# Performance work log

Hardware: AMD Instinct MI355X
Metric: run time of the kernel (lower is better)

Reference implementation:

```python
import jax, jax.numpy as jnp
import numpy as np

DIM = 64
HEADS = 8
P = 4  # polarizations
EPS = 1e-12


def _conv2d(x, w, b, groups):
    # x: [N,C,H,W], w: [O, C//groups, kh, kw] (torch OIHW), stride 1, SAME padding
    y = jax.lax.conv_general_dilated(
        x, w, window_strides=(1, 1), padding='SAME',
        dimension_numbers=('NCHW', 'OIHW', 'NCHW'), feature_group_count=groups)
    return y + b[None, :, None, None]


def setup_inputs() -> dict:
    key = jax.random.key(0)
    ks = jax.random.split(key, 12)
    B, C, H, W = 4, DIM, 128, 128
    s = 1.0 / np.sqrt(C)
    x_in = jax.random.normal(ks[0], (B * P, C, H, W), dtype=jnp.float32)
    mask = jax.random.uniform(ks[1], (B * P, C, H, W), dtype=jnp.float32)
    wq = jax.random.normal(ks[2], (C, C), dtype=jnp.float32) * s
    wk = jax.random.normal(ks[3], (C, C), dtype=jnp.float32) * s
    wv = jax.random.normal(ks[4], (C, C), dtype=jnp.float32) * s
    w_proj = jax.random.normal(ks[5], (C, C), dtype=jnp.float32) * s
    b_proj = jax.random.normal(ks[6], (C,), dtype=jnp.float32) * 0.01
    rescale = jnp.ones((HEADS, 1, 1), dtype=jnp.float32)
    dw_w = jax.random.normal(ks[7], (C, 1, 3, 3), dtype=jnp.float32) * (1.0 / 3.0)
    dw_b = jax.random.normal(ks[8], (C,), dtype=jnp.float32) * 0.01
    pw_w = jax.random.normal(ks[9], (C, C, 1, 1), dtype=jnp.float32) * s
    pw_b = jax.random.normal(ks[10], (C,), dtype=jnp.float32) * 0.01
    return {'x_in': x_in, 'mask': mask, 'wq': wq, 'wk': wk, 'wv': wv,
            'w_proj': w_proj, 'b_proj': b_proj, 'rescale': rescale,
            'dw_w': dw_w, 'dw_b': dw_b, 'pw_w': pw_w, 'pw_b': pw_b}


def reference(x_in, mask, wq, wk, wv, w_proj, b_proj, rescale, dw_w, dw_b, pw_w, pw_b):
    bp, c, h, w = x_in.shape
    b_num = bp // P
    dh = c // HEADS
    # 'b p c h w -> (b h w) p c'
    x = x_in.reshape(b_num, P, c, h, w).transpose(0, 3, 4, 1, 2).reshape(b_num * h * w, P, c)
    # torch Linear (no bias): x @ W.T
    q = jnp.einsum('bpc,dc->bpd', x, wq)
    k = jnp.einsum('bpc,dc->bpd', x, wk)
    v = jnp.einsum('bpc,dc->bpd', x, wv)
    # 'b p (h c) -> b h p c'
    q = q.reshape(-1, P, HEADS, dh).transpose(0, 2, 1, 3)
    k = k.reshape(-1, P, HEADS, dh).transpose(0, 2, 1, 3)
    v = v.reshape(-1, P, HEADS, dh).transpose(0, 2, 1, 3)
    # L2 normalize along head dim (torch F.normalize: clamp_min(eps))
    q = q / jnp.maximum(jnp.linalg.norm(q, axis=-1, keepdims=True), EPS)
    k = k / jnp.maximum(jnp.linalg.norm(k, axis=-1, keepdims=True), EPS)
    atten = jnp.einsum('bhpc,bhqc->bhpq', q, k) * rescale  # rescale: [heads,1,1]
    # mask branch: depthwise 3x3 -> GELU(exact) -> pointwise 1x1
    mg = _conv2d(mask, dw_w, dw_b, groups=c)
    mg = jax.nn.gelu(mg, approximate=False)
    mg = _conv2d(mg, pw_w, pw_b, groups=1)
    mg = mg.reshape(b_num, P, c, h, w).mean(axis=2)  # [b,p,h,w]
    mb = mg.transpose(0, 2, 3, 1).reshape(b_num * h * w, P)  # '(b h w) p'
    mask_bias = mb[:, None, :] - mb[:, :, None]  # [B, p, p]
    atten = atten + mask_bias[:, None, :, :]
    atten = jax.nn.softmax(atten, axis=-1)
    out = jnp.einsum('bhpq,bhqc->bhpc', atten, v)
    out = out.transpose(0, 2, 1, 3).reshape(-1, P, c)  # 'b h p c -> b p (h c)'
    out = jnp.einsum('bpc,dc->bpd', out, w_proj) + b_proj
    # '(b h w) p c -> b p c h w' -> [(b p), c, h, w]
    out = out.reshape(b_num, h, w, P, c).transpose(0, 3, 4, 1, 2)
    return out.reshape(b_num * P, c, h, w)
```

## Files before the change

kernel.cpp:

```cpp
#include <hip/hip_runtime.h>
#include <hip/hip_bf16.h>

#define HSZ 128
#define WSZ 128
#define HWSZ (HSZ*WSZ)
#define NB 4

#define OFF_MB 0

typedef unsigned short u16;
typedef __attribute__((ext_vector_type(8))) short bf16x8;
typedef __attribute__((ext_vector_type(4))) float f32x4;

__device__ __forceinline__ float bf2f(u16 u) {
    return __uint_as_float(((unsigned int)u) << 16);
}
__device__ __forceinline__ unsigned int cvt_pk_bf16(float lo, float hi) {
    __hip_bfloat162 h = __float22bfloat162_rn(make_float2(lo, hi));
    return *(unsigned int*)&h;
}
__device__ __forceinline__ u16 f2bf_bits(float f) {
    unsigned int x = __float_as_uint(f);
    return (u16)((x + 0x7fffu + ((x >> 16) & 1u)) >> 16);
}
__device__ __forceinline__ int sswz(int s) { return s ^ (s >> 3); }
__device__ __forceinline__ int qkv_idx(int t, int d) {
    return (t >> 2)*64 + ((((t & 3) + (t >> 2)) & 3) << 4) + d;
}
__device__ __forceinline__ bf16x8 load_bfrag(const float* W, int drow, int k0) {
    float4 a = *(const float4*)(W + drow*64 + k0);
    float4 b = *(const float4*)(W + drow*64 + k0 + 4);
    unsigned int u[4];
    u[0] = cvt_pk_bf16(a.x, a.y); u[1] = cvt_pk_bf16(a.z, a.w);
    u[2] = cvt_pk_bf16(b.x, b.y); u[3] = cvt_pk_bf16(b.z, b.w);
    return *(bf16x8*)u;
}

__global__ __launch_bounds__(1024) void mask_kernel(const float* __restrict__ mask,
                                                    const float* __restrict__ dww,
                                                    const float* __restrict__ dwb,
                                                    const float* __restrict__ pww,
                                                    float* __restrict__ ws) {
    __shared__ float red[4][256][4];
    __shared__ float cmS[64];
    int tid = threadIdx.x;
    if (tid < 64) {
        float s = 0.f;
        for (int co = 0; co < 64; ++co) s += pww[co*64 + tid];
        cmS[tid] = s * (1.0f/64.0f);
    }
    __syncthreads();
    int bid = blockIdx.x;
    int bp = bid >> 4;
    int hg = bid & 15;
    int cq = tid >> 8;
    int t = tid & 255;
    int h = hg*8 + (t >> 5);
    int w0 = (t & 31) << 2;
    const float* mb_ = mask + (size_t)bp*64*HWSZ;
    int hm = h > 0 ? h-1 : 0;
    int hp = h < 127 ? h+1 : 127;
    float vt = h > 0 ? 1.f : 0.f;
    float vb = h < 127 ? 1.f : 0.f;
    float vl = w0 > 0 ? 1.f : 0.f;
    float vr = w0 < 124 ? 1.f : 0.f;
    int wl = w0 > 0 ? w0-1 : 0;
    int wr = w0 < 124 ? w0+4 : 127;
    float acc0=0.f, acc1=0.f, acc2=0.f, acc3=0.f;
    for (int ci = 0; ci < 16; ++ci) {
        int c = cq*16 + ci;
        const float* rc = mb_ + c*HWSZ;
        const float* r0 = rc + hm*WSZ;
        const float* r1 = rc + h*WSZ;
        const float* r2 = rc + hp*WSZ;
        float4 m0 = *(const float4*)(r0 + w0);
        float4 m1 = *(const float4*)(r1 + w0);
        float4 m2 = *(const float4*)(r2 + w0);
        float L0 = r0[wl]*vl, L1 = r1[wl]*vl, L2 = r2[wl]*vl;
        float R0 = r0[wr]*vr, R1 = r1[wr]*vr, R2 = r2[wr]*vr;
        float w00 = dww[c*9+0]*vt, w01 = dww[c*9+1]*vt, w02 = dww[c*9+2]*vt;
        float w10 = dww[c*9+3],    w11 = dww[c*9+4],    w12 = dww[c*9+5];
        float w20 = dww[c*9+6]*vb, w21 = dww[c*9+7]*vb, w22 = dww[c*9+8]*vb;
        float bb = dwb[c];
        float s0 = bb + w00*L0   + w01*m0.x + w02*m0.y
                      + w10*L1   + w11*m1.x + w12*m1.y
                      + w20*L2   + w21*m2.x + w22*m2.y;
        float s1 = bb + w00*m0.x + w01*m0.y + w02*m0.z
                      + w10*m1.x + w11*m1.y + w12*m1.z
                      + w20*m2.x + w21*m2.y + w22*m2.z;
        float s2 = bb + w00*m0.y + w01*m0.z + w02*m0.w
                      + w10*m1.y + w11*m1.z + w12*m1.w
                      + w20*m2.y + w21*m2.z + w22*m2.w;
        float s3 = bb + w00*m0.z + w01*m0.w + w02*R0
                      + w10*m1.z + w11*m1.w + w12*R1
                      + w20*m2.z + w21*m2.w + w22*R2;
        float cmc = cmS[c];
        acc0 += cmc * (0.5f*s0*(1.f + erff(s0*0.70710678118654752f)));
        acc1 += cmc * (0.5f*s1*(1.f + erff(s1*0.70710678118654752f)));
        acc2 += cmc * (0.5f*s2*(1.f + erff(s2*0.70710678118654752f)));
        acc3 += cmc * (0.5f*s3*(1.f + erff(s3*0.70710678118654752f)));
    }
    red[cq][t][0] = acc0;
    red[cq][t][1] = acc1;
    red[cq][t][2] = acc2;
    red[cq][t][3] = acc3;
    __syncthreads();
    if (tid < 256) {
        int b = bp >> 2, p = bp & 3;
        size_t base = (size_t)b*HWSZ + h*WSZ + w0;
        #pragma unroll
        for (int e = 0; e < 4; ++e) {
            float v = red[0][tid][e] + red[1][tid][e] + red[2][tid][e] + red[3][tid][e];
            ws[OFF_MB + (base+e)*4 + p] = v;
        }
    }
}

__global__ __launch_bounds__(256) void attn_kernel(const float* __restrict__ x_in,
                                                   const float* __restrict__ wq,
                                                   const float* __restrict__ wk,
                                                   const float* __restrict__ wv,
                                                   const float* __restrict__ wp,
                                                   const float* __restrict__ bpj,
                                                   const float* __restrict__ rsc,
                                                   const float* __restrict__ ws,
                                                   float* __restrict__ out) {
    __shared__ u16 smem[32768];
    u16* ldsA = smem;
    u16* ldsQ = smem + 8192;
    u16* ldsK = smem + 16384;
    u16* ldsV = smem + 24576;
    float* outS = (float*)(smem + 8192);

    int t = threadIdx.x;
    int lane = t & 63;
    int wid = __builtin_amdgcn_readfirstlane(t >> 6);
    int n15 = lane & 15;
    int quad = lane >> 4;
    int b = blockIdx.x >> 9;
    int hw0 = (blockIdx.x & 511) << 5;

    bf16x8 fq0 = load_bfrag(wq, wid*16 + n15, quad*8);
    bf16x8 fq1 = load_bfrag(wq, wid*16 + n15, 32 + quad*8);
    bf16x8 fk0 = load_bfrag(wk, wid*16 + n15, quad*8);
    bf16x8 fk1 = load_bfrag(wk, wid*16 + n15, 32 + quad*8);
    bf16x8 fv0 = load_bfrag(wv, wid*16 + n15, quad*8);
    bf16x8 fv1 = load_bfrag(wv, wid*16 + n15, 32 + quad*8);
    bf16x8 fp0 = load_bfrag(wp, wid*16 + n15, quad*8);
    bf16x8 fp1 = load_bfrag(wp, wid*16 + n15, 32 + quad*8);
    float bias = bpj[wid*16 + n15];

    unsigned int* ldsA32 = (unsigned int*)ldsA;
    for (int it = 0; it < 4; ++it) {
        int i = t + (it << 8);
        int rp = i >> 3, l4 = i & 7;
        int p = rp >> 5, cp = rp & 31;
        int c0 = cp*2;
        const float* r0 = x_in + (size_t)(b*256 + p*64 + c0)*HWSZ + hw0 + l4*4;
        float4 v0 = *(const float4*)r0;
        float4 v1 = *(const float4*)(r0 + HWSZ);
        int kt = c0 >> 5, qd = (c0 >> 3) & 3, j2 = (c0 & 7) >> 1;
        float a0[4] = {v0.x, v0.y, v0.z, v0.w};
        float a1[4] = {v1.x, v1.y, v1.z, v1.w};
        #pragma unroll
        for (int e = 0; e < 4; ++e) {
            int tau = (p << 5) + (l4 << 2) + e;
            int slot = (tau & 15) | (qd << 4);
            ldsA32[((tau >> 4)*2 + kt)*256 + sswz(slot)*4 + j2] = cvt_pk_bf16(a0[e], a1[e]);
        }
    }
    __syncthreads();

    int sl8 = sswz(lane)*8;
    for (int mt = 0; mt < 8; ++mt) {
        bf16x8 a0 = *(const bf16x8*)(ldsA + mt*1024 + sl8);
        bf16x8 a1 = *(const bf16x8*)(ldsA + mt*1024 + 512 + sl8);
        f32x4 aq = {0.f,0.f,0.f,0.f};
        f32x4 ak = {0.f,0.f,0.f,0.f};
        f32x4 av = {0.f,0.f,0.f,0.f};
        aq = __builtin_amdgcn_mfma_f32_16x16x32_bf16(a0, fq0, aq, 0, 0, 0);
        aq = __builtin_amdgcn_mfma_f32_16x16x32_bf16(a1, fq1, aq, 0, 0, 0);
        ak = __builtin_amdgcn_mfma_f32_16x16x32_bf16(a0, fk0, ak, 0, 0, 0);
        ak = __builtin_amdgcn_mfma_f32_16x16x32_bf16(a1, fk1, ak, 0, 0, 0);
        av = __builtin_amdgcn_mfma_f32_16x16x32_bf16(a0, fv0, av, 0, 0, 0);
        av = __builtin_amdgcn_mfma_f32_16x16x32_bf16(a1, fv1, av, 0, 0, 0);
        int tb = (mt*4 + wid)*256;
        #pragma unroll
        for (int r = 0; r < 4; ++r) {
            int idx = tb + quad*64 + ((((r + quad) & 3)) << 4) + n15;
            ldsQ[idx] = f2bf_bits(aq[r]);
            ldsK[idx] = f2bf_bits(ak[r]);
            ldsV[idx] = f2bf_bits(av[r]);
        }
    }
    __syncthreads();

    {
        int pix = t & 31;
        int hd = t >> 5;
        float qv[4][8], kv[4][8], vv[4][8];
        #pragma unroll
        for (int p = 0; p < 4; ++p) {
            int tau = (p << 5) + pix;
            int base = ((tau >> 4)*4 + (hd >> 1))*256 + qkv_idx(tau & 15, (hd & 1)*8);
            bf16x8 q8 = *(const bf16x8*)(ldsQ + base);
            bf16x8 k8 = *(const bf16x8*)(ldsK + base);
            bf16x8 v8 = *(const bf16x8*)(ldsV + base);
            #pragma unroll
            for (int j = 0; j < 8; ++j) {
                qv[p][j] = bf2f((u16)q8[j]);
                kv[p][j] = bf2f((u16)k8[j]);
                vv[p][j] = bf2f((u16)v8[j]);
            }
        }
        #pragma unroll
        for (int p = 0; p < 4; ++p) {
            float sq = 0.f, sk = 0.f;
            #pragma unroll
            for (int j = 0; j < 8; ++j) { sq += qv[p][j]*qv[p][j]; sk += kv[p][j]*kv[p][j]; }
            float iq = 1.0f / fmaxf(sqrtf(sq), 1e-12f);
            float ik = 1.0f / fmaxf(sqrtf(sk), 1e-12f);
            #pragma unroll
            for (int j = 0; j < 8; ++j) { qv[p][j] *= iq; kv[p][j] *= ik; }
        }
        float4 mb4 = *(const float4*)(ws + OFF_MB + ((size_t)b*HWSZ + hw0 + pix)*4);
        float mba[4] = {mb4.x, mb4.y, mb4.z, mb4.w};
        float rs = rsc[hd];
        float at[4][4];
        #pragma unroll
        for (int p = 0; p < 4; ++p) {
            #pragma unroll
            for (int r = 0; r < 4; ++r) {
                float d = 0.f;
                #pragma unroll
                for (int j = 0; j < 8; ++j) d += qv[p][j]*kv[r][j];
                at[p][r] = d*rs + mba[r];
            }
            float m = fmaxf(fmaxf(at[p][0], at[p][1]), fmaxf(at[p][2], at[p][3]));
            float e0 = expf(at[p][0]-m), e1 = expf(at[p][1]-m);
            float e2 = expf(at[p][2]-m), e3 = expf(at[p][3]-m);
            float inv = 1.0f / (e0+e1+e2+e3);
            at[p][0]=e0*inv; at[p][1]=e1*inv; at[p][2]=e2*inv; at[p][3]=e3*inv;
        }
        unsigned int* ldsA32w = (unsigned int*)ldsA;
        #pragma unroll
        for (int p = 0; p < 4; ++p) {
            float y[8];
            #pragma unroll
            for (int j = 0; j < 8; ++j) {
                y[j] = at[p][0]*vv[0][j] + at[p][1]*vv[1][j]
                     + at[p][2]*vv[2][j] + at[p][3]*vv[3][j];
            }
            int tau = (p << 5) + pix;
            int slot = (tau & 15) | ((hd & 3) << 4);
            unsigned int pk[4];
            pk[0] = cvt_pk_bf16(y[0], y[1]); pk[1] = cvt_pk_bf16(y[2], y[3]);
            pk[2] = cvt_pk_bf16(y[4], y[5]); pk[3] = cvt_pk_bf16(y[6], y[7]);
            *(uint4*)(ldsA32w + ((tau >> 4)*2 + (hd >> 2))*256 + sswz(slot)*4) = *(uint4*)pk;
        }
    }
    __syncthreads();

    for (int mt = 0; mt < 8; ++mt) {
        bf16x8 a0 = *(const bf16x8*)(ldsA + mt*1024 + sl8);
        bf16x8 a1 = *(const bf16x8*)(ldsA + mt*1024 + 512 + sl8);
        f32x4 ao = {0.f,0.f,0.f,0.f};
        ao = __builtin_amdgcn_mfma_f32_16x16x32_bf16(a0, fp0, ao, 0, 0, 0);
        ao = __builtin_amdgcn_mfma_f32_16x16x32_bf16(a1, fp1, ao, 0, 0, 0);
        #pragma unroll
        for (int r = 0; r < 4; ++r) {
            int tau = mt*16 + quad*4 + r;
            int d = wid*16 + n15;
            outS[tau*64 + (d ^ (tau & 31))] = ao[r] + bias;
        }
    }
    __syncthreads();
    for (int g = 0; g < 32; ++g) {
        int flat = (g << 8) + t;
        int px = flat & 31;
        int pd = flat >> 5;
        int d = pd & 63;
        int p = pd >> 6;
        int tau = (p << 5) + px;
        out[(size_t)((b*4 + p)*64 + d)*HWSZ + hw0 + px] = outS[tau*64 + (d ^ (tau & 31))];
    }
}

extern "C" void kernel_launch(void* const* d_in, const int* in_sizes, int n_in,
                              void* d_out, int out_size, void* d_ws, size_t ws_size,
                              hipStream_t stream) {
    const float* x_in  = (const float*)d_in[0];
    const float* mask  = (const float*)d_in[1];
    const float* wq    = (const float*)d_in[2];
    const float* wk    = (const float*)d_in[3];
    const float* wv    = (const float*)d_in[4];
    const float* wproj = (const float*)d_in[5];
    const float* bproj = (const float*)d_in[6];
    const float* resc  = (const float*)d_in[7];
    const float* dww   = (const float*)d_in[8];
    const float* dwb   = (const float*)d_in[9];
    const float* pww   = (const float*)d_in[10];
    float* ws = (float*)d_ws;
    float* outp = (float*)d_out;

    hipLaunchKernelGGL(mask_kernel, dim3(256), dim3(1024), 0, stream,
                       mask, dww, dwb, pww, ws);
    hipLaunchKernelGGL(attn_kernel, dim3(2048), dim3(256), 0, stream,
                       x_in, wq, wk, wv, wproj, bproj, resc, ws, outp);
}
```

Before: 236.5 us.

## Double attention block threads to 512 and vectorize output stores

```diff
diff --git a/kernel.cpp b/kernel.cpp
--- a/kernel.cpp
+++ b/kernel.cpp
@@ -116,15 +116,15 @@
     }
 }
 
-__global__ __launch_bounds__(256) void attn_kernel(const float* __restrict__ x_in,
-                                                   const float* __restrict__ wq,
-                                                   const float* __restrict__ wk,
-                                                   const float* __restrict__ wv,
-                                                   const float* __restrict__ wp,
-                                                   const float* __restrict__ bpj,
-                                                   const float* __restrict__ rsc,
-                                                   const float* __restrict__ ws,
-                                                   float* __restrict__ out) {
+__global__ __launch_bounds__(512, 4) void attn_kernel(const float* __restrict__ x_in,
+                                                      const float* __restrict__ wq,
+                                                      const float* __restrict__ wk,
+                                                      const float* __restrict__ wv,
+                                                      const float* __restrict__ wp,
+                                                      const float* __restrict__ bpj,
+                                                      const float* __restrict__ rsc,
+                                                      const float* __restrict__ ws,
+                                                      float* __restrict__ out) {
     __shared__ u16 smem[32768];
     u16* ldsA = smem;
     u16* ldsQ = smem + 8192;
@@ -135,24 +135,26 @@
     int t = threadIdx.x;
     int lane = t & 63;
     int wid = __builtin_amdgcn_readfirstlane(t >> 6);
+    int dq = wid & 3;
+    int half = wid >> 2;
     int n15 = lane & 15;
     int quad = lane >> 4;
     int b = blockIdx.x >> 9;
     int hw0 = (blockIdx.x & 511) << 5;
 
-    bf16x8 fq0 = load_bfrag(wq, wid*16 + n15, quad*8);
-    bf16x8 fq1 = load_bfrag(wq, wid*16 + n15, 32 + quad*8);
-    bf16x8 fk0 = load_bfrag(wk, wid*16 + n15, quad*8);
-    bf16x8 fk1 = load_bfrag(wk, wid*16 + n15, 32 + quad*8);
-    bf16x8 fv0 = load_bfrag(wv, wid*16 + n15, quad*8);
-    bf16x8 fv1 = load_bfrag(wv, wid*16 + n15, 32 + quad*8);
-    bf16x8 fp0 = load_bfrag(wp, wid*16 + n15, quad*8);
-    bf16x8 fp1 = load_bfrag(wp, wid*16 + n15, 32 + quad*8);
-    float bias = bpj[wid*16 + n15];
+    bf16x8 fq0 = load_bfrag(wq, dq*16 + n15, quad*8);
+    bf16x8 fq1 = load_bfrag(wq, dq*16 + n15, 32 + quad*8);
+    bf16x8 fk0 = load_bfrag(wk, dq*16 + n15, quad*8);
+    bf16x8 fk1 = load_bfrag(wk, dq*16 + n15, 32 + quad*8);
+    bf16x8 fv0 = load_bfrag(wv, dq*16 + n15, quad*8);
+    bf16x8 fv1 = load_bfrag(wv, dq*16 + n15, 32 + quad*8);
+    bf16x8 fp0 = load_bfrag(wp, dq*16 + n15, quad*8);
+    bf16x8 fp1 = load_bfrag(wp, dq*16 + n15, 32 + quad*8);
+    float bias = bpj[dq*16 + n15];
 
     unsigned int* ldsA32 = (unsigned int*)ldsA;
-    for (int it = 0; it < 4; ++it) {
-        int i = t + (it << 8);
+    for (int it = 0; it < 2; ++it) {
+        int i = t + (it << 9);
         int rp = i >> 3, l4 = i & 7;
         int p = rp >> 5, cp = rp & 31;
         int c0 = cp*2;
@@ -172,7 +174,8 @@
     __syncthreads();
 
     int sl8 = sswz(lane)*8;
-    for (int mt = 0; mt < 8; ++mt) {
+    for (int m = 0; m < 4; ++m) {
+        int mt = (half << 2) + m;
         bf16x8 a0 = *(const bf16x8*)(ldsA + mt*1024 + sl8);
         bf16x8 a1 = *(const bf16x8*)(ldsA + mt*1024 + 512 + sl8);
         f32x4 aq = {0.f,0.f,0.f,0.f};
@@ -184,7 +187,7 @@
         ak = __builtin_amdgcn_mfma_f32_16x16x32_bf16(a1, fk1, ak, 0, 0, 0);
         av = __builtin_amdgcn_mfma_f32_16x16x32_bf16(a0, fv0, av, 0, 0, 0);
         av = __builtin_amdgcn_mfma_f32_16x16x32_bf16(a1, fv1, av, 0, 0, 0);
-        int tb = (mt*4 + wid)*256;
+        int tb = (mt*4 + dq)*256;
         #pragma unroll
         for (int r = 0; r < 4; ++r) {
             int idx = tb + quad*64 + ((((r + quad) & 3)) << 4) + n15;
@@ -197,59 +200,72 @@
 
     {
         int pix = t & 31;
-        int hd = t >> 5;
-        float qv[4][8], kv[4][8], vv[4][8];
+        int hd = (t >> 5) & 7;
+        int ph = t >> 8;
+        float qv[2][8], kv[4][8], vv[4][8];
         #pragma unroll
         for (int p = 0; p < 4; ++p) {
             int tau = (p << 5) + pix;
             int base = ((tau >> 4)*4 + (hd >> 1))*256 + qkv_idx(tau & 15, (hd & 1)*8);
-            bf16x8 q8 = *(const bf16x8*)(ldsQ + base);
             bf16x8 k8 = *(const bf16x8*)(ldsK + base);
             bf16x8 v8 = *(const bf16x8*)(ldsV + base);
             #pragma unroll
             for (int j = 0; j < 8; ++j) {
-                qv[p][j] = bf2f((u16)q8[j]);
                 kv[p][j] = bf2f((u16)k8[j]);
                 vv[p][j] = bf2f((u16)v8[j]);
             }
         }
         #pragma unroll
+        for (int pq = 0; pq < 2; ++pq) {
+            int tau = (((ph << 1) + pq) << 5) + pix;
+            int base = ((tau >> 4)*4 + (hd >> 1))*256 + qkv_idx(tau & 15, (hd & 1)*8);
+            bf16x8 q8 = *(const bf16x8*)(ldsQ + base);
+            #pragma unroll
+            for (int j = 0; j < 8; ++j) qv[pq][j] = bf2f((u16)q8[j]);
+        }
+        #pragma unroll
         for (int p = 0; p < 4; ++p) {
-            float sq = 0.f, sk = 0.f;
-            #pragma unroll
-            for (int j = 0; j < 8; ++j) { sq += qv[p][j]*qv[p][j]; sk += kv[p][j]*kv[p][j]; }
+            float sk = 0.f;
+            #pragma unroll
+            for (int j = 0; j < 8; ++j) sk += kv[p][j]*kv[p][j];
+            float ik = 1.0f / fmaxf(sqrtf(sk), 1e-12f);
+            #pragma unroll
+            for (int j = 0; j < 8; ++j) kv[p][j] *= ik;
+        }
+        #pragma unroll
+        for (int pq = 0; pq < 2; ++pq) {
+            float sq = 0.f;
+            #pragma unroll
+            for (int j = 0; j < 8; ++j) sq += qv[pq][j]*qv[pq][j];
             float iq = 1.0f / fmaxf(sqrtf(sq), 1e-12f);
-            float ik = 1.0f / fmaxf(sqrtf(sk), 1e-12f);
-            #pragma unroll
-            for (int j = 0; j < 8; ++j) { qv[p][j] *= iq; kv[p][j] *= ik; }
+            #pragma unroll
+            for (int j = 0; j < 8; ++j) qv[pq][j] *= iq;
         }
         float4 mb4 = *(const float4*)(ws + OFF_MB + ((size_t)b*HWSZ + hw0 + pix)*4);
         float mba[4] = {mb4.x, mb4.y, mb4.z, mb4.w};
         float rs = rsc[hd];
-        float at[4][4];
-        #pragma unroll
-        for (int p = 0; p < 4; ++p) {
+        unsigned int* ldsA32w = (unsigned int*)ldsA;
+        #pragma unroll
+        for (int pq = 0; pq < 2; ++pq) {
+            int p = (ph << 1) + pq;
+            float at[4];
             #pragma unroll
             for (int r = 0; r < 4; ++r) {
                 float d = 0.f;
                 #pragma unroll
-                for (int j = 0; j < 8; ++j) d += qv[p][j]*kv[r][j];
-                at[p][r] = d*rs + mba[r];
+                for (int j = 0; j < 8; ++j) d += qv[pq][j]*kv[r][j];
+                at[r] = d*rs + mba[r];
             }
-            float m = fmaxf(fmaxf(at[p][0], at[p][1]), fmaxf(at[p][2], at[p][3]));
-            float e0 = expf(at[p][0]-m), e1 = expf(at[p][1]-m);
-            float e2 = expf(at[p][2]-m), e3 = expf(at[p][3]-m);
+            float m = fmaxf(fmaxf(at[0], at[1]), fmaxf(at[2], at[3]));
+            float e0 = __expf(at[0]-m), e1 = __expf(at[1]-m);
+            float e2 = __expf(at[2]-m), e3 = __expf(at[3]-m);
             float inv = 1.0f / (e0+e1+e2+e3);
-            at[p][0]=e0*inv; at[p][1]=e1*inv; at[p][2]=e2*inv; at[p][3]=e3*inv;
-        }
-        unsigned int* ldsA32w = (unsigned int*)ldsA;
-        #pragma unroll
-        for (int p = 0; p < 4; ++p) {
+            at[0]=e0*inv; at[1]=e1*inv; at[2]=e2*inv; at[3]=e3*inv;
             float y[8];
             #pragma unroll
             for (int j = 0; j < 8; ++j) {
-                y[j] = at[p][0]*vv[0][j] + at[p][1]*vv[1][j]
-                     + at[p][2]*vv[2][j] + at[p][3]*vv[3][j];
+                y[j] = at[0]*vv[0][j] + at[1]*vv[1][j]
+                     + at[2]*vv[2][j] + at[3]*vv[3][j];
             }
             int tau = (p << 5) + pix;
             int slot = (tau & 15) | ((hd & 3) << 4);
@@ -261,7 +277,8 @@
     }
     __syncthreads();
 
-    for (int mt = 0; mt < 8; ++mt) {
+    for (int m = 0; m < 4; ++m) {
+        int mt = (half << 2) + m;
         bf16x8 a0 = *(const bf16x8*)(ldsA + mt*1024 + sl8);
         bf16x8 a1 = *(const bf16x8*)(ldsA + mt*1024 + 512 + sl8);
         f32x4 ao = {0.f,0.f,0.f,0.f};
@@ -270,19 +287,25 @@
         #pragma unroll
         for (int r = 0; r < 4; ++r) {
             int tau = mt*16 + quad*4 + r;
-            int d = wid*16 + n15;
+            int d = dq*16 + n15;
             outS[tau*64 + (d ^ (tau & 31))] = ao[r] + bias;
         }
     }
     __syncthreads();
-    for (int g = 0; g < 32; ++g) {
-        int flat = (g << 8) + t;
-        int px = flat & 31;
-        int pd = flat >> 5;
+    #pragma unroll
+    for (int g = 0; g < 4; ++g) {
+        int flat = (g << 9) + t;
+        int px = (flat & 7) << 2;
+        int pd = flat >> 3;
         int d = pd & 63;
         int p = pd >> 6;
-        int tau = (p << 5) + px;
-        out[(size_t)((b*4 + p)*64 + d)*HWSZ + hw0 + px] = outS[tau*64 + (d ^ (tau & 31))];
+        int tb0 = (p << 5) + px;
+        float4 o;
+        o.x = outS[(tb0+0)*64 + (d ^ ((tb0+0) & 31))];
+        o.y = outS[(tb0+1)*64 + (d ^ ((tb0+1) & 31))];
+        o.z = outS[(tb0+2)*64 + (d ^ ((tb0+2) & 31))];
+        o.w = outS[(tb0+3)*64 + (d ^ ((tb0+3) & 31))];
+        *(float4*)(out + (size_t)((b*4 + p)*64 + d)*HWSZ + hw0 + px) = o;
     }
 }
 
@@ -305,6 +328,6 @@
 
     hipLaunchKernelGGL(mask_kernel, dim3(256), dim3(1024), 0, stream,
                        mask, dww, dwb, pww, ws);
-    hipLaunchKernelGGL(attn_kernel, dim3(2048), dim3(256), 0, stream,
+    hipLaunchKernelGGL(attn_kernel, dim3(2048), dim3(512), 0, stream,
                        x_in, wq, wk, wv, wproj, bproj, resc, ws, outp);
 }
```

New measurement: 239.2 us. No clear change (+1.1%).

## Restructure attention kernel: smaller tiles, per-lane attention with shuffles, direct output stores

Applied to the files above, without the earlier changes.

```diff
diff --git a/kernel.cpp b/kernel.cpp
--- a/kernel.cpp
+++ b/kernel.cpp
@@ -19,14 +19,7 @@
     __hip_bfloat162 h = __float22bfloat162_rn(make_float2(lo, hi));
     return *(unsigned int*)&h;
 }
-__device__ __forceinline__ u16 f2bf_bits(float f) {
-    unsigned int x = __float_as_uint(f);
-    return (u16)((x + 0x7fffu + ((x >> 16) & 1u)) >> 16);
-}
 __device__ __forceinline__ int sswz(int s) { return s ^ (s >> 3); }
-__device__ __forceinline__ int qkv_idx(int t, int d) {
-    return (t >> 2)*64 + ((((t & 3) + (t >> 2)) & 3) << 4) + d;
-}
 __device__ __forceinline__ bf16x8 load_bfrag(const float* W, int drow, int k0) {
     float4 a = *(const float4*)(W + drow*64 + k0);
     float4 b = *(const float4*)(W + drow*64 + k0 + 4);
@@ -116,173 +109,155 @@
     }
 }
 
-__global__ __launch_bounds__(256) void attn_kernel(const float* __restrict__ x_in,
-                                                   const float* __restrict__ wq,
-                                                   const float* __restrict__ wk,
-                                                   const float* __restrict__ wv,
-                                                   const float* __restrict__ wp,
-                                                   const float* __restrict__ bpj,
-                                                   const float* __restrict__ rsc,
-                                                   const float* __restrict__ ws,
-                                                   float* __restrict__ out) {
-    __shared__ u16 smem[32768];
+__global__ __launch_bounds__(512, 8) void attn_kernel(const float* __restrict__ x_in,
+                                                      const float* __restrict__ wq,
+                                                      const float* __restrict__ wk,
+                                                      const float* __restrict__ wv,
+                                                      const float* __restrict__ wp,
+                                                      const float* __restrict__ bpj,
+                                                      const float* __restrict__ rsc,
+                                                      const float* __restrict__ ws,
+                                                      float* __restrict__ out) {
+    __shared__ u16 smem[16384];
     u16* ldsA = smem;
-    u16* ldsQ = smem + 8192;
-    u16* ldsK = smem + 16384;
-    u16* ldsV = smem + 24576;
-    float* outS = (float*)(smem + 8192);
+    u16* ldsQ = smem + 4096;
+    u16* ldsK = smem + 8192;
+    u16* ldsV = smem + 12288;
+    unsigned int* ldsA32 = (unsigned int*)ldsA;
 
     int t = threadIdx.x;
     int lane = t & 63;
     int wid = __builtin_amdgcn_readfirstlane(t >> 6);
+    int dq = wid & 3;
+    int half = wid >> 2;
     int n15 = lane & 15;
     int quad = lane >> 4;
-    int b = blockIdx.x >> 9;
-    int hw0 = (blockIdx.x & 511) << 5;
-
-    bf16x8 fq0 = load_bfrag(wq, wid*16 + n15, quad*8);
-    bf16x8 fq1 = load_bfrag(wq, wid*16 + n15, 32 + quad*8);
-    bf16x8 fk0 = load_bfrag(wk, wid*16 + n15, quad*8);
-    bf16x8 fk1 = load_bfrag(wk, wid*16 + n15, 32 + quad*8);
-    bf16x8 fv0 = load_bfrag(wv, wid*16 + n15, quad*8);
-    bf16x8 fv1 = load_bfrag(wv, wid*16 + n15, 32 + quad*8);
-    bf16x8 fp0 = load_bfrag(wp, wid*16 + n15, quad*8);
-    bf16x8 fp1 = load_bfrag(wp, wid*16 + n15, 32 + quad*8);
-    float bias = bpj[wid*16 + n15];
-
-    unsigned int* ldsA32 = (unsigned int*)ldsA;
-    for (int it = 0; it < 4; ++it) {
-        int i = t + (it << 8);
-        int rp = i >> 3, l4 = i & 7;
+    int b = blockIdx.x >> 10;
+    int hw0 = (blockIdx.x & 1023) << 4;
+
+    bf16x8 fq0 = load_bfrag(wq, dq*16 + n15, quad*8);
+    bf16x8 fq1 = load_bfrag(wq, dq*16 + n15, 32 + quad*8);
+    bf16x8 fk0 = load_bfrag(wk, dq*16 + n15, quad*8);
+    bf16x8 fk1 = load_bfrag(wk, dq*16 + n15, 32 + quad*8);
+    bf16x8 fv0 = load_bfrag(wv, dq*16 + n15, quad*8);
+    bf16x8 fv1 = load_bfrag(wv, dq*16 + n15, 32 + quad*8);
+
+    {
+        int rp = t >> 2, l4 = t & 3;
         int p = rp >> 5, cp = rp & 31;
         int c0 = cp*2;
         const float* r0 = x_in + (size_t)(b*256 + p*64 + c0)*HWSZ + hw0 + l4*4;
         float4 v0 = *(const float4*)r0;
         float4 v1 = *(const float4*)(r0 + HWSZ);
         int kt = c0 >> 5, qd = (c0 >> 3) & 3, j2 = (c0 & 7) >> 1;
-        float a0[4] = {v0.x, v0.y, v0.z, v0.w};
-        float a1[4] = {v1.x, v1.y, v1.z, v1.w};
+        float a0v[4] = {v0.x, v0.y, v0.z, v0.w};
+        float a1v[4] = {v1.x, v1.y, v1.z, v1.w};
         #pragma unroll
         for (int e = 0; e < 4; ++e) {
-            int tau = (p << 5) + (l4 << 2) + e;
+            int tau = (p << 4) + (l4 << 2) + e;
             int slot = (tau & 15) | (qd << 4);
-            ldsA32[((tau >> 4)*2 + kt)*256 + sswz(slot)*4 + j2] = cvt_pk_bf16(a0[e], a1[e]);
+            ldsA32[((tau >> 4)*2 + kt)*256 + sswz(slot)*4 + j2] = cvt_pk_bf16(a0v[e], a1v[e]);
         }
     }
     __syncthreads();
 
     int sl8 = sswz(lane)*8;
-    for (int mt = 0; mt < 8; ++mt) {
+    for (int m = 0; m < 2; ++m) {
+        int mt = half*2 + m;
         bf16x8 a0 = *(const bf16x8*)(ldsA + mt*1024 + sl8);
         bf16x8 a1 = *(const bf16x8*)(ldsA + mt*1024 + 512 + sl8);
         f32x4 aq = {0.f,0.f,0.f,0.f};
         f32x4 ak = {0.f,0.f,0.f,0.f};
         f32x4 av = {0.f,0.f,0.f,0.f};
-        aq = __builtin_amdgcn_mfma_f32_16x16x32_bf16(a0, fq0, aq, 0, 0, 0);
-        aq = __builtin_amdgcn_mfma_f32_16x16x32_bf16(a1, fq1, aq, 0, 0, 0);
-        ak = __builtin_amdgcn_mfma_f32_16x16x32_bf16(a0, fk0, ak, 0, 0, 0);
-        ak = __builtin_amdgcn_mfma_f32_16x16x32_bf16(a1, fk1, ak, 0, 0, 0);
-        av = __builtin_amdgcn_mfma_f32_16x16x32_bf16(a0, fv0, av, 0, 0, 0);
-        av = __builtin_amdgcn_mfma_f32_16x16x32_bf16(a1, fv1, av, 0, 0, 0);
-        int tb = (mt*4 + wid)*256;
-        #pragma unroll
-        for (int r = 0; r < 4; ++r) {
-            int idx = tb + quad*64 + ((((r + quad) & 3)) << 4) + n15;
-            ldsQ[idx] = f2bf_bits(aq[r]);
-            ldsK[idx] = f2bf_bits(ak[r]);
-            ldsV[idx] = f2bf_bits(av[r]);
-        }
+        aq = __builtin_amdgcn_mfma_f32_16x16x32_bf16(fq0, a0, aq, 0, 0, 0);
+        aq = __builtin_amdgcn_mfma_f32_16x16x32_bf16(fq1, a1, aq, 0, 0, 0);
+        ak = __builtin_amdgcn_mfma_f32_16x16x32_bf16(fk0, a0, ak, 0, 0, 0);
+        ak = __builtin_amdgcn_mfma_f32_16x16x32_bf16(fk1, a1, ak, 0, 0, 0);
+        av = __builtin_amdgcn_mfma_f32_16x16x32_bf16(fv0, a0, av, 0, 0, 0);
+        av = __builtin_amdgcn_mfma_f32_16x16x32_bf16(fv1, a1, av, 0, 0, 0);
+        int tg = mt*16 + n15;
+        int g = ((dq << 2) + quad) ^ ((n15 & 7) << 1);
+        int off = tg*64 + g*4;
+        uint2 pq, pk, pv;
+        pq.x = cvt_pk_bf16(aq[0], aq[1]); pq.y = cvt_pk_bf16(aq[2], aq[3]);
+        pk.x = cvt_pk_bf16(ak[0], ak[1]); pk.y = cvt_pk_bf16(ak[2], ak[3]);
+        pv.x = cvt_pk_bf16(av[0], av[1]); pv.y = cvt_pk_bf16(av[2], av[3]);
+        *(uint2*)(ldsQ + off) = pq;
+        *(uint2*)(ldsK + off) = pk;
+        *(uint2*)(ldsV + off) = pv;
     }
     __syncthreads();
 
     {
-        int pix = t & 31;
-        int hd = t >> 5;
-        float qv[4][8], kv[4][8], vv[4][8];
-        #pragma unroll
-        for (int p = 0; p < 4; ++p) {
-            int tau = (p << 5) + pix;
-            int base = ((tau >> 4)*4 + (hd >> 1))*256 + qkv_idx(tau & 15, (hd & 1)*8);
-            bf16x8 q8 = *(const bf16x8*)(ldsQ + base);
-            bf16x8 k8 = *(const bf16x8*)(ldsK + base);
-            bf16x8 v8 = *(const bf16x8*)(ldsV + base);
-            #pragma unroll
-            for (int j = 0; j < 8; ++j) {
-                qv[p][j] = bf2f((u16)q8[j]);
-                kv[p][j] = bf2f((u16)k8[j]);
-                vv[p][j] = bf2f((u16)v8[j]);
-            }
-        }
-        #pragma unroll
-        for (int p = 0; p < 4; ++p) {
-            float sq = 0.f, sk = 0.f;
-            #pragma unroll
-            for (int j = 0; j < 8; ++j) { sq += qv[p][j]*qv[p][j]; sk += kv[p][j]*kv[p][j]; }
-            float iq = 1.0f / fmaxf(sqrtf(sq), 1e-12f);
-            float ik = 1.0f / fmaxf(sqrtf(sk), 1e-12f);
-            #pragma unroll
-            for (int j = 0; j < 8; ++j) { qv[p][j] *= iq; kv[p][j] *= ik; }
-        }
-        float4 mb4 = *(const float4*)(ws + OFF_MB + ((size_t)b*HWSZ + hw0 + pix)*4);
-        float mba[4] = {mb4.x, mb4.y, mb4.z, mb4.w};
-        float rs = rsc[hd];
-        float at[4][4];
-        #pragma unroll
-        for (int p = 0; p < 4; ++p) {
-            #pragma unroll
-            for (int r = 0; r < 4; ++r) {
-                float d = 0.f;
-                #pragma unroll
-                for (int j = 0; j < 8; ++j) d += qv[p][j]*kv[r][j];
-                at[p][r] = d*rs + mba[r];
-            }
-            float m = fmaxf(fmaxf(at[p][0], at[p][1]), fmaxf(at[p][2], at[p][3]));
-            float e0 = expf(at[p][0]-m), e1 = expf(at[p][1]-m);
-            float e2 = expf(at[p][2]-m), e3 = expf(at[p][3]-m);
-            float inv = 1.0f / (e0+e1+e2+e3);
-            at[p][0]=e0*inv; at[p][1]=e1*inv; at[p][2]=e2*inv; at[p][3]=e3*inv;
-        }
-        unsigned int* ldsA32w = (unsigned int*)ldsA;
-        #pragma unroll
-        for (int p = 0; p < 4; ++p) {
-            float y[8];
-            #pragma unroll
-            for (int j = 0; j < 8; ++j) {
-                y[j] = at[p][0]*vv[0][j] + at[p][1]*vv[1][j]
-                     + at[p][2]*vv[2][j] + at[p][3]*vv[3][j];
-            }
-            int tau = (p << 5) + pix;
-            int slot = (tau & 15) | ((hd & 3) << 4);
-            unsigned int pk[4];
-            pk[0] = cvt_pk_bf16(y[0], y[1]); pk[1] = cvt_pk_bf16(y[2], y[3]);
-            pk[2] = cvt_pk_bf16(y[4], y[5]); pk[3] = cvt_pk_bf16(y[6], y[7]);
-            *(uint4*)(ldsA32w + ((tau >> 4)*2 + (hd >> 2))*256 + sswz(slot)*4) = *(uint4*)pk;
-        }
-    }
-    __syncthreads();
-
-    for (int mt = 0; mt < 8; ++mt) {
+        int p = t & 3;
+        int hd = (t >> 2) & 7;
+        int pix = t >> 5;
+        int token = (p << 4) + pix;
+        int off = token*64 + ((hd ^ (pix & 7)) << 3);
+        bf16x8 q8 = *(const bf16x8*)(ldsQ + off);
+        bf16x8 k8 = *(const bf16x8*)(ldsK + off);
+        bf16x8 v8 = *(const bf16x8*)(ldsV + off);
+        float qv[8], kv[8];
+        float sq = 0.f, sk = 0.f;
+        #pragma unroll
+        for (int j = 0; j < 8; ++j) {
+            qv[j] = bf2f((u16)q8[j]);
+            kv[j] = bf2f((u16)k8[j]);
+            sq += qv[j]*qv[j];
+            sk += kv[j]*kv[j];
+        }
+        float iq = rsqrtf(fmaxf(sq, 1e-24f));
+        float ik = rsqrtf(fmaxf(sk, 1e-24f));
+        float d0 = 0.f, d1 = 0.f, d2 = 0.f, d3 = 0.f;
+        #pragma unroll
+        for (int j = 0; j < 8; ++j) {
+            float kj = kv[j];
+            d0 += qv[j]*kj;
+            d1 += qv[j]*__shfl_xor(kj, 1);
+            d2 += qv[j]*__shfl_xor(kj, 2);
+            d3 += qv[j]*__shfl_xor(kj, 3);
+        }
+        float mbp = ws[OFF_MB + ((size_t)b*HWSZ + hw0 + pix)*4 + p];
+        float iqrs = iq * rsc[hd];
+        float s0 = d0*(iqrs*ik)                 + mbp;
+        float s1 = d1*(iqrs*__shfl_xor(ik, 1))  + __shfl_xor(mbp, 1);
+        float s2 = d2*(iqrs*__shfl_xor(ik, 2))  + __shfl_xor(mbp, 2);
+        float s3 = d3*(iqrs*__shfl_xor(ik, 3))  + __shfl_xor(mbp, 3);
+        float mx = fmaxf(fmaxf(s0, s1), fmaxf(s2, s3));
+        float e0 = __expf(s0-mx), e1 = __expf(s1-mx);
+        float e2 = __expf(s2-mx), e3 = __expf(s3-mx);
+        float inv = 1.0f / (e0+e1+e2+e3);
+        float w0 = e0*inv, w1 = e1*inv, w2 = e2*inv, w3 = e3*inv;
+        float y[8];
+        #pragma unroll
+        for (int j = 0; j < 8; ++j) {
+            float vj = bf2f((u16)v8[j]);
+            y[j] = w0*vj + w1*__shfl_xor(vj, 1)
+                 + w2*__shfl_xor(vj, 2) + w3*__shfl_xor(vj, 3);
+        }
+        unsigned int pk4[4];
+        pk4[0] = cvt_pk_bf16(y[0], y[1]); pk4[1] = cvt_pk_bf16(y[2], y[3]);
+        pk4[2] = cvt_pk_bf16(y[4], y[5]); pk4[3] = cvt_pk_bf16(y[6], y[7]);
+        int slot = pix | ((hd & 3) << 4);
+        *(uint4*)(ldsA32 + (p*2 + (hd >> 2))*256 + sswz(slot)*4) = *(uint4*)pk4;
+    }
+    __syncthreads();
+
+    bf16x8 fp0 = load_bfrag(wp, dq*16 + n15, quad*8);
+    bf16x8 fp1 = load_bfrag(wp, dq*16 + n15, 32 + quad*8);
+    float4 b4 = *(const float4*)(bpj + dq*16 + quad*4);
+    for (int m = 0; m < 2; ++m) {
+        int mt = half*2 + m;
         bf16x8 a0 = *(const bf16x8*)(ldsA + mt*1024 + sl8);
         bf16x8 a1 = *(const bf16x8*)(ldsA + mt*1024 + 512 + sl8);
         f32x4 ao = {0.f,0.f,0.f,0.f};
-        ao = __builtin_amdgcn_mfma_f32_16x16x32_bf16(a0, fp0, ao, 0, 0, 0);
-        ao = __builtin_amdgcn_mfma_f32_16x16x32_bf16(a1, fp1, ao, 0, 0, 0);
-        #pragma unroll
-        for (int r = 0; r < 4; ++r) {
-            int tau = mt*16 + quad*4 + r;
-            int d = wid*16 + n15;
-            outS[tau*64 + (d ^ (tau & 31))] = ao[r] + bias;
-        }
-    }
-    __syncthreads();
-    for (int g = 0; g < 32; ++g) {
-        int flat = (g << 8) + t;
-        int px = flat & 31;
-        int pd = flat >> 5;
-        int d = pd & 63;
-        int p = pd >> 6;
-        int tau = (p << 5) + px;
-        out[(size_t)((b*4 + p)*64 + d)*HWSZ + hw0 + px] = outS[tau*64 + (d ^ (tau & 31))];
+        ao = __builtin_amdgcn_mfma_f32_16x16x32_bf16(fp0, a0, ao, 0, 0, 0);
+        ao = __builtin_amdgcn_mfma_f32_16x16x32_bf16(fp1, a1, ao, 0, 0, 0);
+        size_t obase = ((size_t)((b*4 + mt)*64 + dq*16 + quad*4))*HWSZ + hw0 + n15;
+        out[obase]          = ao[0] + b4.x;
+        out[obase +   HWSZ] = ao[1] + b4.y;
+        out[obase + 2*HWSZ] = ao[2] + b4.z;
+        out[obase + 3*HWSZ] = ao[3] + b4.w;
     }
 }
 
@@ -305,6 +280,6 @@
 
     hipLaunchKernelGGL(mask_kernel, dim3(256), dim3(1024), 0, stream,
                        mask, dww, dwb, pww, ws);
-    hipLaunchKernelGGL(attn_kernel, dim3(2048), dim3(256), 0, stream,
+    hipLaunchKernelGGL(attn_kernel, dim3(4096), dim3(512), 0, stream,
                        x_in, wq, wk, wv, wproj, bproj, resc, ws, outp);
 }
```

After: 268.2 us. 1.13x slower.
